# Kernel tuning notes

Measured on AMD Instinct MI355X. Metric: run time of the kernel, lower is better.

The kernel has to match this reference:

```python
import jax, jax.numpy as jnp
import numpy as np

N = 100000   # nodes
E = 600000   # edges
D = 128      # hidden_dim
R = 8        # edge_vocab_size (num_relations)
B = 64       # graphs in batch
V = 5000     # node_vocab_size
L = 3        # num_layers


def setup_inputs() -> dict:
    key = jax.random.key(0)
    ks = jax.random.split(key, 16)
    s = 1.0 / np.sqrt(D)
    node_type = jax.random.randint(ks[0], (N,), 0, V, dtype=jnp.int32)
    edge_index = jax.random.randint(ks[1], (2, E), 0, N, dtype=jnp.int32)
    edge_type = jax.random.randint(ks[2], (E,), 0, R, dtype=jnp.int32)
    batch = jnp.sort(jax.random.randint(ks[3], (N,), 0, B, dtype=jnp.int32))
    node_emb = jax.random.normal(ks[4], (V, D), dtype=jnp.float32)
    rel_w = jax.random.normal(ks[5], (L, R, D, D), dtype=jnp.float32) * s
    root_w = jax.random.normal(ks[6], (L, D, D), dtype=jnp.float32) * s
    bias = jnp.zeros((L, D), dtype=jnp.float32)
    risk_w1 = jax.random.normal(ks[7], (D, D), dtype=jnp.float32) * s
    risk_b1 = jnp.zeros((D,), dtype=jnp.float32)
    risk_w2 = jax.random.normal(ks[8], (D, 1), dtype=jnp.float32) * s
    risk_b2 = jnp.zeros((1,), dtype=jnp.float32)
    safe_w1 = jax.random.normal(ks[9], (D, D), dtype=jnp.float32) * s
    safe_b1 = jnp.zeros((D,), dtype=jnp.float32)
    safe_w2 = jax.random.normal(ks[10], (D, 1), dtype=jnp.float32) * s
    safe_b2 = jnp.zeros((1,), dtype=jnp.float32)
    return dict(node_type=node_type, edge_index=edge_index, edge_type=edge_type,
                batch=batch, node_emb=node_emb, rel_w=rel_w, root_w=root_w,
                bias=bias, risk_w1=risk_w1, risk_b1=risk_b1, risk_w2=risk_w2,
                risk_b2=risk_b2, safe_w1=safe_w1, safe_b1=safe_b1,
                safe_w2=safe_w2, safe_b2=safe_b2)


def _rgcn_layer(x, edge_index, edge_type, Wrel, Wroot, b):
    # PyG RGCNConv: per-relation mean aggregation of source features,
    # then relation-specific linear + root transform + bias.
    src, dst = edge_index[0], edge_index[1]
    seg = dst * R + edge_type                      # combined (node, relation) id
    msgs = x[src]                                  # [E, D] gather
    sums = jax.ops.segment_sum(msgs, seg, num_segments=N * R)      # [N*R, D]
    cnt = jax.ops.segment_sum(jnp.ones((E,), x.dtype), seg, num_segments=N * R)
    mean = sums / jnp.maximum(cnt, 1.0)[:, None]
    mean = mean.reshape(N, R, D)
    out = jnp.einsum('nrd,rde->ne', mean, Wrel) + x @ Wroot + b
    return out


def _mlp_head(g, w1, b1, w2, b2):
    h = jax.nn.relu(g @ w1 + b1)
    return (h @ w2 + b2).squeeze(-1)               # dropout is identity in eval


def reference(node_type, edge_index, edge_type, batch, node_emb, rel_w, root_w,
              bias, risk_w1, risk_b1, risk_w2, risk_b2, safe_w1, safe_b1,
              safe_w2, safe_b2):
    x = node_emb[node_type]                        # [N, D]
    for l in range(L):                             # fixed small layer loop
        x = jax.nn.relu(_rgcn_layer(x, edge_index, edge_type,
                                    rel_w[l], root_w[l], bias[l]))
    # global_mean_pool over graph ids
    g_sum = jax.ops.segment_sum(x, batch, num_segments=B)          # [B, D]
    g_cnt = jax.ops.segment_sum(jnp.ones((N,), x.dtype), batch, num_segments=B)
    g = g_sum / jnp.maximum(g_cnt, 1.0)[:, None]
    risk_pred = _mlp_head(g, risk_w1, risk_b1, risk_w2, risk_b2)   # [B]
    safe_logit = _mlp_head(g, safe_w1, safe_b1, safe_w2, safe_b2)  # [B]
    return risk_pred, safe_logit
```

## Files before the change

### kernel.cpp

```cpp
#include <hip/hip_runtime.h>
#include <hip/hip_bf16.h>

#define N_NODES 100000
#define N_EDGES 600000
#define DIM     128
#define N_REL   8
#define N_GRAPH 64
#define N_LAYER 3
#define NR      (N_NODES * N_REL)
#define NB1     782

typedef __attribute__((ext_vector_type(4))) float float4v;
typedef __attribute__((ext_vector_type(2))) float float2v;
typedef unsigned long long ull;

__device__ __forceinline__ int gswz8(int row, int g) {
    return row * 16 + (g ^ (row & 15));
}

__global__ void k_hist(const int* __restrict__ ei, const int* __restrict__ et,
                       int* __restrict__ counts) {
    int e = blockIdx.x * 256 + threadIdx.x;
    if (e < N_EDGES) {
        int seg = ei[N_EDGES + e] * N_REL + et[e];
        atomicAdd(&counts[seg], 1);
    }
}

__global__ __launch_bounds__(256) void k_scan1(const int* __restrict__ cnts,
                                               int* __restrict__ part,
                                               int* __restrict__ bsum) {
    __shared__ int sh[256];
    int t = threadIdx.x;
    int base = blockIdx.x * 1024 + t * 4;
    int v0 = (base + 0 < NR) ? cnts[base + 0] : 0;
    int v1 = (base + 1 < NR) ? cnts[base + 1] : 0;
    int v2 = (base + 2 < NR) ? cnts[base + 2] : 0;
    int v3 = (base + 3 < NR) ? cnts[base + 3] : 0;
    int tot = v0 + v1 + v2 + v3;
    sh[t] = tot;
    __syncthreads();
    for (int off = 1; off < 256; off <<= 1) {
        int x = (t >= off) ? sh[t - off] : 0;
        __syncthreads();
        sh[t] += x;
        __syncthreads();
    }
    int exc = sh[t] - tot;
    if (base + 0 < NR) part[base + 0] = exc;
    if (base + 1 < NR) part[base + 1] = exc + v0;
    if (base + 2 < NR) part[base + 2] = exc + v0 + v1;
    if (base + 3 < NR) part[base + 3] = exc + v0 + v1 + v2;
    if (t == 255) bsum[blockIdx.x] = sh[t];
}

__global__ __launch_bounds__(1024) void k_scan2(int* __restrict__ bsum, int nb) {
    __shared__ int sh[1024];
    int t = threadIdx.x;
    int v = (t < nb) ? bsum[t] : 0;
    sh[t] = v;
    __syncthreads();
    for (int off = 1; off < 1024; off <<= 1) {
        int x = (t >= off) ? sh[t - off] : 0;
        __syncthreads();
        sh[t] += x;
        __syncthreads();
    }
    if (t < nb) bsum[t] = sh[t] - v;
}

__global__ void k_scan3(const int* __restrict__ part, const int* __restrict__ bsum,
                        int* __restrict__ rowptr, int* __restrict__ cursor) {
    int i = blockIdx.x * 256 + threadIdx.x;
    if (i < NR) {
        int v = part[i] + bsum[i >> 10];
        rowptr[i] = v;
        cursor[i] = v;
    }
    if (i == 0) rowptr[NR] = N_EDGES;
}

__global__ void k_scatter(const int* __restrict__ ei, const int* __restrict__ et,
                          int* __restrict__ cursor, int* __restrict__ srcs) {
    int e = blockIdx.x * 256 + threadIdx.x;
    if (e < N_EDGES) {
        int seg = ei[N_EDGES + e] * N_REL + et[e];
        int p = atomicAdd(&cursor[seg], 1);
        srcs[p] = ei[e];
    }
}

__global__ void k_gather8(const int* __restrict__ nt, const float* __restrict__ emb,
                          unsigned int* __restrict__ x8) {
    int gid = blockIdx.x * 256 + threadIdx.x;
    if (gid < N_NODES * 32) {
        int n = gid >> 5, up = gid & 31;
        const float* row = emb + (size_t)nt[n] * DIM;
        int p0 = up * 4;
        float f0 = row[((p0 + 0) & 7) * 16 + ((p0 + 0) >> 3)];
        float f1 = row[((p0 + 1) & 7) * 16 + ((p0 + 1) >> 3)];
        float f2 = row[((p0 + 2) & 7) * 16 + ((p0 + 2) >> 3)];
        float f3 = row[((p0 + 3) & 7) * 16 + ((p0 + 3) >> 3)];
        int u = __builtin_amdgcn_cvt_pk_fp8_f32(f0, f1, 0, false);
        u = __builtin_amdgcn_cvt_pk_fp8_f32(f2, f3, u, true);
        x8[gid] = (unsigned int)u;
    }
}

#define W8_TOTAL (N_LAYER * 9 * 8192)
__global__ void k_wprep9(const float* __restrict__ relw, const float* __restrict__ rootw,
                         unsigned short* __restrict__ W8) {
    int gid = blockIdx.x * 256 + threadIdx.x;
    if (gid < W8_TOTAL) {
        int l = gid / (9 * 8192);
        int rem = gid - l * 9 * 8192;
        int r = rem >> 13;
        int idx = rem & 8191;
        int n = idx >> 6, p2 = idx & 63;
        int pos0 = 2 * p2, pos1 = 2 * p2 + 1;
        int k0 = (pos0 & 7) * 16 + (pos0 >> 3);
        int k1 = (pos1 & 7) * 16 + (pos1 >> 3);
        float w0, w1;
        if (r < 8) {
            const float* base = relw + ((size_t)(l * 8 + r) * 128) * 128 + n;
            w0 = base[(size_t)k0 * 128];
            w1 = base[(size_t)k1 * 128];
        } else {
            const float* base = rootw + (size_t)l * 128 * 128 + n;
            w0 = base[(size_t)k0 * 128];
            w1 = base[(size_t)k1 * 128];
        }
        int pk = __builtin_amdgcn_cvt_pk_fp8_f32(w0, w1, 0, false);
        W8[gid] = (unsigned short)(pk & 0xffff);
    }
}

__global__ __launch_bounds__(256) void k_agg(
    const unsigned int* __restrict__ x8,
    const int* __restrict__ rowptr,
    const int* __restrict__ srcs,
    unsigned int* __restrict__ Ag8,
    int d0, int rows, int srows)
{
    const int t = threadIdx.x;
    const int wv = t >> 6, lane = t & 63;
    const int q = lane >> 4, j = lane & 15;
    const int nb0 = (blockIdx.x * 4 + wv) * 4;
    if (nb0 >= rows) return;
    const int myn = nb0 + q;
    const bool nvalid = (myn < rows);

    int pr = 0;
    {
        int idx = (d0 + nb0) * 8 + lane;
        if (idx > NR) idx = NR;
        if (lane < 33) pr = rowptr[idx];
    }
    const int P0 = __shfl(pr, 0);
    const int Dtot = __shfl(pr, 32) - P0;

    int my_src = 0;
    if (lane < Dtot) my_src = srcs[P0 + lane];

    const uint2* x2p = (const uint2*)x8;

    for (int r = 0; r < 8; ++r) {
        int e0 = __shfl(pr, q * 8 + r);
        int e1 = __shfl(pr, q * 8 + r + 1);
        int cnt = e1 - e0;
        int m1 = max(cnt, __shfl_xor(cnt, 16));
        int maxc = max(m1, __shfl_xor(m1, 32));
        float2v A0 = {0.f, 0.f}, A1 = {0.f, 0.f}, A2 = {0.f, 0.f}, A3 = {0.f, 0.f};
        int k = 0;
        for (; k + 2 <= maxc; k += 2) {
            int ei0 = e0 + k, ei1 = e0 + k + 1;
            int r0 = ei0 - P0, r1 = ei1 - P0;
            int s0 = __shfl(my_src, r0 & 63);
            int s1 = __shfl(my_src, r1 & 63);
            if (r0 >= 64) s0 = srcs[ei0];
            if (r1 >= 64) s1 = srcs[ei1];
            bool v0 = (k < cnt), v1 = (k + 1 < cnt);
            uint2 u0, u1;
            if (v0) u0 = x2p[(size_t)s0 * 16 + j];
            if (v1) u1 = x2p[(size_t)s1 * 16 + j];
            if (v0) {
                A0 += __builtin_amdgcn_cvt_pk_f32_fp8((int)u0.x, false);
                A1 += __builtin_amdgcn_cvt_pk_f32_fp8((int)u0.x, true);
                A2 += __builtin_amdgcn_cvt_pk_f32_fp8((int)u0.y, false);
                A3 += __builtin_amdgcn_cvt_pk_f32_fp8((int)u0.y, true);
            }
            if (v1) {
                A0 += __builtin_amdgcn_cvt_pk_f32_fp8((int)u1.x, false);
                A1 += __builtin_amdgcn_cvt_pk_f32_fp8((int)u1.x, true);
                A2 += __builtin_amdgcn_cvt_pk_f32_fp8((int)u1.y, false);
                A3 += __builtin_amdgcn_cvt_pk_f32_fp8((int)u1.y, true);
            }
        }
        if (k < maxc) {
            int ei = e0 + k;
            int ridx = ei - P0;
            int s = __shfl(my_src, ridx & 63);
            if (ridx >= 64) s = srcs[ei];
            if (k < cnt) {
                uint2 u = x2p[(size_t)s * 16 + j];
                A0 += __builtin_amdgcn_cvt_pk_f32_fp8((int)u.x, false);
                A1 += __builtin_amdgcn_cvt_pk_f32_fp8((int)u.x, true);
                A2 += __builtin_amdgcn_cvt_pk_f32_fp8((int)u.y, false);
                A3 += __builtin_amdgcn_cvt_pk_f32_fp8((int)u.y, true);
            }
        }
        float inv = (cnt > 0) ? 1.0f / (float)cnt : 0.f;
        float2v iv = {inv, inv};
        A0 *= iv; A1 *= iv; A2 *= iv; A3 *= iv;
        int u0 = __builtin_amdgcn_cvt_pk_fp8_f32(A0.x, A0.y, 0, false);
        u0 = __builtin_amdgcn_cvt_pk_fp8_f32(A1.x, A1.y, u0, true);
        int u1 = __builtin_amdgcn_cvt_pk_fp8_f32(A2.x, A2.y, 0, false);
        u1 = __builtin_amdgcn_cvt_pk_fp8_f32(A3.x, A3.y, u1, true);
        if (nvalid) {
            uint2 v; v.x = (unsigned int)u0; v.y = (unsigned int)u1;
            *(uint2*)&Ag8[((size_t)r * srows + myn) * 32 + j * 2] = v;
        }
    }
}

#define BM2 128
__global__ __launch_bounds__(256) void k_gemm(
    const unsigned int* __restrict__ Ag8,
    const unsigned int* __restrict__ x8in,
    unsigned int* __restrict__ x8out,
    const unsigned short* __restrict__ W8,
    const float* __restrict__ bias,
    int d0, int srows)
{
    __shared__ __align__(16) ull Als[4096];
    __shared__ __align__(16) ull Bls[4096];
    const int t = threadIdx.x;
    const int wv = t >> 6, lane = t & 63;
    const int quad = lane >> 4, l15 = lane & 15;
    const int m0 = d0 + blockIdx.x * BM2;

    float4v acc[2][8];
#pragma unroll
    for (int nt = 0; nt < 8; ++nt) {
        float bc = bias[nt * 16 + l15];
        acc[0][nt] = (float4v){bc, bc, bc, bc};
        acc[1][nt] = (float4v){bc, bc, bc, bc};
    }

    const ull* Abase = (const ull*)Ag8 + (size_t)(m0 - d0) * 16;
    const size_t cstride = (size_t)srows * 16;
    const ull* Aroot = (const ull*)x8in + (size_t)m0 * 16;

    ull aR[8], bR[8];
    {
        const ull* Ac = Abase;
        const ull* Wc = (const ull*)W8;
#pragma unroll
        for (int i = 0; i < 8; ++i) {
            aR[i] = Ac[t + 256 * i];
            bR[i] = Wc[t + 256 * i];
        }
    }
#pragma unroll
    for (int i = 0; i < 8; ++i) {
        int idx = t + 256 * i;
        int sw = gswz8(idx >> 4, idx & 15);
        Als[sw] = aR[i];
        Bls[sw] = bR[i];
    }
    __syncthreads();

    for (int c = 0; c < 9; ++c) {
        const int cur = (c & 1) * 2048;
        if (c < 8) {
            const ull* Ac = (c + 1 < 8) ? (Abase + (size_t)(c + 1) * cstride) : Aroot;
            const ull* Wc = (const ull*)(W8 + (size_t)(c + 1) * 8192);
#pragma unroll
            for (int i = 0; i < 8; ++i) {
                aR[i] = Ac[t + 256 * i];
                bR[i] = Wc[t + 256 * i];
            }
        }
#pragma unroll
        for (int kk = 0; kk < 4; ++kk) {
            int g = kk * 4 + quad;
            long long a0 = (long long)Als[cur + (wv * 32 + l15) * 16 + (g ^ l15)];
            long long a1 = (long long)Als[cur + (wv * 32 + 16 + l15) * 16 + (g ^ l15)];
#pragma unroll
            for (int nt = 0; nt < 8; ++nt) {
                long long b8 = (long long)Bls[cur + (nt * 16 + l15) * 16 + (g ^ l15)];
                acc[0][nt] = __builtin_amdgcn_mfma_f32_16x16x32_fp8_fp8(a0, b8, acc[0][nt], 0, 0, 0);
                acc[1][nt] = __builtin_amdgcn_mfma_f32_16x16x32_fp8_fp8(a1, b8, acc[1][nt], 0, 0, 0);
            }
        }
        if (c < 8) {
            const int nxt = ((c + 1) & 1) * 2048;
#pragma unroll
            for (int i = 0; i < 8; ++i) {
                int idx = t + 256 * i;
                int sw = gswz8(idx >> 4, idx & 15);
                Als[nxt + sw] = aR[i];
                Bls[nxt + sw] = bR[i];
            }
            __syncthreads();
        }
    }
    ull* outs = (ull*)x8out;
#pragma unroll
    for (int rt = 0; rt < 2; ++rt) {
#pragma unroll
        for (int i = 0; i < 4; ++i) {
            int row = m0 + wv * 32 + rt * 16 + quad * 4 + i;
            float v0 = acc[rt][0][i], v1 = acc[rt][1][i];
            float v2 = acc[rt][2][i], v3 = acc[rt][3][i];
            float v4 = acc[rt][4][i], v5 = acc[rt][5][i];
            float v6 = acc[rt][6][i], v7 = acc[rt][7][i];
            v0 = v0 > 0.f ? v0 : 0.f;  v1 = v1 > 0.f ? v1 : 0.f;
            v2 = v2 > 0.f ? v2 : 0.f;  v3 = v3 > 0.f ? v3 : 0.f;
            v4 = v4 > 0.f ? v4 : 0.f;  v5 = v5 > 0.f ? v5 : 0.f;
            v6 = v6 > 0.f ? v6 : 0.f;  v7 = v7 > 0.f ? v7 : 0.f;
            int lo = __builtin_amdgcn_cvt_pk_fp8_f32(v0, v1, 0, false);
            lo = __builtin_amdgcn_cvt_pk_fp8_f32(v2, v3, lo, true);
            int hi = __builtin_amdgcn_cvt_pk_fp8_f32(v4, v5, 0, false);
            hi = __builtin_amdgcn_cvt_pk_fp8_f32(v6, v7, hi, true);
            if (row < N_NODES) {
                ull w = ((ull)(unsigned int)hi << 32) | (unsigned int)lo;
                outs[(size_t)row * 16 + l15] = w;
            }
        }
    }
}

__global__ __launch_bounds__(256) void k_pool(const unsigned int* __restrict__ x8,
                                              const int* __restrict__ batch,
                                              float* __restrict__ gsum,
                                              int* __restrict__ gcnt) {
    const int wv = threadIdx.x >> 6, lane = threadIdx.x & 63;
    const int n0 = (blockIdx.x * 4 + wv) * 64;
    if (n0 >= N_NODES) return;
    int n1 = n0 + 64;
    if (n1 > N_NODES) n1 = N_NODES;
    const int nb = n1 - n0;
    const unsigned short* xs = (const unsigned short*)x8;
    int bb = batch[n0 + (lane < nb ? lane : nb - 1)];
    float2v A = {0.f, 0.f};
    int run = 0;
    int cur = __shfl(bb, 0);
    for (int base = 0; base < nb; base += 8) {
        unsigned int u[8];
        int m = nb - base;
#pragma unroll
        for (int qq = 0; qq < 8; ++qq)
            if (qq < m) u[qq] = xs[(size_t)(n0 + base + qq) * 64 + lane];
#pragma unroll
        for (int qq = 0; qq < 8; ++qq) {
            if (qq < m) {
                int b = __shfl(bb, base + qq);
                if (b != cur) {
                    atomicAdd(&gsum[cur * 128 + lane * 2], A.x);
                    atomicAdd(&gsum[cur * 128 + lane * 2 + 1], A.y);
                    if (lane == 0) atomicAdd(&gcnt[cur], run);
                    A = (float2v){0.f, 0.f};
                    run = 0;
                    cur = b;
                }
                A += __builtin_amdgcn_cvt_pk_f32_fp8((int)u[qq], false);
                ++run;
            }
        }
    }
    atomicAdd(&gsum[cur * 128 + lane * 2], A.x);
    atomicAdd(&gsum[cur * 128 + lane * 2 + 1], A.y);
    if (lane == 0) atomicAdd(&gcnt[cur], run);
}

__global__ __launch_bounds__(128) void k_heads(
    const float* __restrict__ gsum, const int* __restrict__ gcnt,
    const float* __restrict__ rw1, const float* __restrict__ rb1,
    const float* __restrict__ rw2, const float* __restrict__ rb2,
    const float* __restrict__ sw1, const float* __restrict__ sb1,
    const float* __restrict__ sw2, const float* __restrict__ sb2,
    float* __restrict__ out) {
    __shared__ float g[128];
    __shared__ float parts[2];
    int b = blockIdx.x, t = threadIdx.x;
    int c = gcnt[b];
    float invc = 1.0f / (float)(c > 0 ? c : 1);
    g[((t & 7) << 4) | (t >> 3)] = gsum[b * 128 + t] * invc;
    __syncthreads();
    float acc = rb1[t];
    for (int d = 0; d < 128; ++d) acc += g[d] * rw1[d * 128 + t];
    float h = acc > 0.f ? acc : 0.f;
    float p = h * rw2[t];
    for (int o = 32; o > 0; o >>= 1) p += __shfl_down(p, o);
    if ((t & 63) == 0) parts[t >> 6] = p;
    __syncthreads();
    if (t == 0) out[b] = parts[0] + parts[1] + rb2[0];
    __syncthreads();
    acc = sb1[t];
    for (int d = 0; d < 128; ++d) acc += g[d] * sw1[d * 128 + t];
    h = acc > 0.f ? acc : 0.f;
    p = h * sw2[t];
    for (int o = 32; o > 0; o >>= 1) p += __shfl_down(p, o);
    if ((t & 63) == 0) parts[t >> 6] = p;
    __syncthreads();
    if (t == 0) out[64 + b] = parts[0] + parts[1] + sb2[0];
}

extern "C" void kernel_launch(void* const* d_in, const int* in_sizes, int n_in,
                              void* d_out, int out_size, void* d_ws, size_t ws_size,
                              hipStream_t stream) {
    const int*   node_type  = (const int*)d_in[0];
    const int*   edge_index = (const int*)d_in[1];
    const int*   edge_type  = (const int*)d_in[2];
    const int*   batch      = (const int*)d_in[3];
    const float* node_emb   = (const float*)d_in[4];
    const float* rel_w      = (const float*)d_in[5];
    const float* root_w     = (const float*)d_in[6];
    const float* bias       = (const float*)d_in[7];
    const float* rw1        = (const float*)d_in[8];
    const float* rb1        = (const float*)d_in[9];
    const float* rw2        = (const float*)d_in[10];
    const float* rb2        = (const float*)d_in[11];
    const float* sw1        = (const float*)d_in[12];
    const float* sb1        = (const float*)d_in[13];
    const float* sw2        = (const float*)d_in[14];
    const float* sb2        = (const float*)d_in[15];
    float* out = (float*)d_out;

    char* ws = (char*)d_ws;
    size_t off = 0;
    auto alloc = [&](size_t bytes) -> void* {
        void* p = ws + off;
        off += (bytes + 255) & ~(size_t)255;
        return p;
    };
    unsigned int*   x8a    = (unsigned int*)alloc((size_t)N_NODES * 32 * 4);
    unsigned int*   x8b    = (unsigned int*)alloc((size_t)N_NODES * 32 * 4);
    int*            rowptr = (int*)alloc((size_t)(NR + 1) * 4);
    int*            srcs   = (int*)alloc((size_t)N_EDGES * 4);
    int*            bsum   = (int*)alloc(1024 * 4);
    unsigned short* W8     = (unsigned short*)alloc((size_t)W8_TOTAL * 2);
    float*          gsum   = (float*)alloc((64 * 128 + 64) * 4);
    int*            gcnt   = (int*)(gsum + 64 * 128);
    size_t off_common = off;
    int*            cursor = (int*)alloc((size_t)NR * 4);
    int*            counts = (int*)alloc((size_t)NR * 4);
    size_t off_sort = off;
    if (off_sort > ws_size) return;
    unsigned int*   Ag8    = (unsigned int*)(ws + off_common);
    size_t avail = ws_size - off_common;
    long max_rows = (avail > 32768) ? (long)((avail - 32768) / 1024) : 0;
    int srows = (int)((max_rows / 64) * 64);
    if (srows > N_NODES + 63) srows = ((N_NODES + 63) / 64) * 64;
    if (srows < 128) return;

    hipMemsetAsync(counts, 0, (size_t)NR * 4, stream);
    hipMemsetAsync(gsum, 0, (size_t)(64 * 128 + 64) * 4, stream);
    k_hist<<<(N_EDGES + 255) / 256, 256, 0, stream>>>(edge_index, edge_type, counts);
    k_scan1<<<NB1, 256, 0, stream>>>(counts, cursor, bsum);
    k_scan2<<<1, 1024, 0, stream>>>(bsum, NB1);
    k_scan3<<<(NR + 255) / 256, 256, 0, stream>>>(cursor, bsum, rowptr, cursor);
    k_scatter<<<(N_EDGES + 255) / 256, 256, 0, stream>>>(edge_index, edge_type, cursor, srcs);

    k_gather8<<<(N_NODES * 32 + 255) / 256, 256, 0, stream>>>(node_type, node_emb, x8a);
    k_wprep9<<<(W8_TOTAL + 255) / 256, 256, 0, stream>>>(rel_w, root_w, W8);

    unsigned int* xcur = x8a;
    unsigned int* xnext = x8b;
    for (int l = 0; l < N_LAYER; ++l) {
        const unsigned short* W8l = W8 + (size_t)l * 9 * 8192;
        const float* bl = bias + (size_t)l * 128;
        for (int d0 = 0; d0 < N_NODES; d0 += srows) {
            int rows = N_NODES - d0;
            if (rows > srows) rows = srows;
            int ab = (rows + 15) / 16;
            int gb = (rows + BM2 - 1) / BM2;
            k_agg<<<ab, 256, 0, stream>>>(xcur, rowptr, srcs, Ag8, d0, rows, srows);
            k_gemm<<<gb, 256, 0, stream>>>(Ag8, xcur, xnext, W8l, bl, d0, srows);
        }
        unsigned int* tmp = xcur; xcur = xnext; xnext = tmp;
    }

    k_pool<<<(N_NODES + 255) / 256, 256, 0, stream>>>(xcur, batch, gsum, gcnt);
    k_heads<<<64, 128, 0, stream>>>(gsum, gcnt, rw1, rb1, rw2, rb2,
                                    sw1, sb1, sw2, sb2, out);
}
```

Baseline: 427.6 us.

## Write aggregated features in MFMA fragment layout and load A directly to registers

The aggregation kernel now stores its per-relation mean features in a 16-row tiled layout that matches the MFMA A-operand fragment order. The GEMM kernel then loads A fragments straight from global memory into registers, with a register double buffer, and drops the shared-memory A tile and its swizzled stores. The root-feature chunk is gathered per lane from the row-major x8 array. This removes LDS traffic and shared memory use for A, but each wave loads its own A fragments with less coalescing on the root chunk.

```diff
diff --git a/kernel.cpp b/kernel.cpp
--- a/kernel.cpp
+++ b/kernel.cpp
@@ -163,6 +163,7 @@
     if (lane < Dtot) my_src = srcs[P0 + lane];
 
     const uint2* x2p = (const uint2*)x8;
+    uint2* Agf = (uint2*)Ag8;
 
     for (int r = 0; r < 8; ++r) {
         int e0 = __shfl(pr, q * 8 + r);
@@ -218,7 +219,7 @@
         u1 = __builtin_amdgcn_cvt_pk_fp8_f32(A3.x, A3.y, u1, true);
         if (nvalid) {
             uint2 v; v.x = (unsigned int)u0; v.y = (unsigned int)u1;
-            *(uint2*)&Ag8[((size_t)r * srows + myn) * 32 + j * 2] = v;
+            Agf[(size_t)r * srows * 16 + (size_t)(myn >> 4) * 256 + j * 16 + (myn & 15)] = v;
         }
     }
 }
@@ -232,7 +233,6 @@
     const float* __restrict__ bias,
     int d0, int srows)
 {
-    __shared__ __align__(16) ull Als[4096];
     __shared__ __align__(16) ull Bls[4096];
     const int t = threadIdx.x;
     const int wv = t >> 6, lane = t & 63;
@@ -247,45 +247,50 @@
         acc[1][nt] = (float4v){bc, bc, bc, bc};
     }
 
-    const ull* Abase = (const ull*)Ag8 + (size_t)(m0 - d0) * 16;
-    const size_t cstride = (size_t)srows * 16;
-    const ull* Aroot = (const ull*)x8in + (size_t)m0 * 16;
-
-    ull aR[8], bR[8];
+    const size_t pstride = (size_t)srows * 16;
+    const ull* Ag = (const ull*)Ag8 + ((size_t)((m0 - d0) >> 4) + 2 * wv) * 256;
+    const ull* Xr = (const ull*)x8in;
+
+    ull aC[8], aN[8], bR[8];
     {
-        const ull* Ac = Abase;
         const ull* Wc = (const ull*)W8;
 #pragma unroll
         for (int i = 0; i < 8; ++i) {
-            aR[i] = Ac[t + 256 * i];
+            aC[i] = Ag[(size_t)(i >> 2) * 256 + (i & 3) * 64 + lane];
             bR[i] = Wc[t + 256 * i];
         }
     }
 #pragma unroll
     for (int i = 0; i < 8; ++i) {
         int idx = t + 256 * i;
-        int sw = gswz8(idx >> 4, idx & 15);
-        Als[sw] = aR[i];
-        Bls[sw] = bR[i];
+        Bls[gswz8(idx >> 4, idx & 15)] = bR[i];
     }
     __syncthreads();
 
     for (int c = 0; c < 9; ++c) {
         const int cur = (c & 1) * 2048;
         if (c < 8) {
-            const ull* Ac = (c + 1 < 8) ? (Abase + (size_t)(c + 1) * cstride) : Aroot;
+            if (c + 1 < 8) {
+                const ull* Ac = Ag + (size_t)(c + 1) * pstride;
+#pragma unroll
+                for (int i = 0; i < 8; ++i)
+                    aN[i] = Ac[(size_t)(i >> 2) * 256 + (i & 3) * 64 + lane];
+            } else {
+#pragma unroll
+                for (int i = 0; i < 8; ++i) {
+                    int rt = i >> 2, kk = i & 3;
+                    aN[i] = Xr[(size_t)(m0 + wv * 32 + rt * 16 + l15) * 16 + kk * 4 + quad];
+                }
+            }
             const ull* Wc = (const ull*)(W8 + (size_t)(c + 1) * 8192);
 #pragma unroll
-            for (int i = 0; i < 8; ++i) {
-                aR[i] = Ac[t + 256 * i];
-                bR[i] = Wc[t + 256 * i];
-            }
+            for (int i = 0; i < 8; ++i) bR[i] = Wc[t + 256 * i];
         }
 #pragma unroll
         for (int kk = 0; kk < 4; ++kk) {
+            long long a0 = (long long)aC[kk];
+            long long a1 = (long long)aC[4 + kk];
             int g = kk * 4 + quad;
-            long long a0 = (long long)Als[cur + (wv * 32 + l15) * 16 + (g ^ l15)];
-            long long a1 = (long long)Als[cur + (wv * 32 + 16 + l15) * 16 + (g ^ l15)];
 #pragma unroll
             for (int nt = 0; nt < 8; ++nt) {
                 long long b8 = (long long)Bls[cur + (nt * 16 + l15) * 16 + (g ^ l15)];
@@ -298,9 +303,8 @@
 #pragma unroll
             for (int i = 0; i < 8; ++i) {
                 int idx = t + 256 * i;
-                int sw = gswz8(idx >> 4, idx & 15);
-                Als[nxt + sw] = aR[i];
-                Bls[nxt + sw] = bR[i];
+                Bls[nxt + gswz8(idx >> 4, idx & 15)] = bR[i];
+                aC[i] = aN[i];
             }
             __syncthreads();
         }
```

Measured after the change: 421.9 us. About the same (-1.3%).
